# Performance work log

Hardware: AMD Instinct MI355X
Metric: run time of the kernel (lower is better)

Reference implementation:

```python
import jax, jax.numpy as jnp
import numpy as np

LN_EPS = 1e-5


def setup_inputs() -> dict:
    key = jax.random.key(0)
    ks = jax.random.split(key, 4)
    B, D, N = 256, 1024, 100000
    scale = 1.0 / np.sqrt(D)
    return {
        "query": jax.random.normal(ks[0], (B, D), dtype=jnp.float32),
        "W1": jax.random.normal(ks[1], (D, D), dtype=jnp.float32) * scale,
        "b1": jnp.zeros((D,), dtype=jnp.float32),
        "ln_g": jnp.ones((D,), dtype=jnp.float32),
        "ln_b": jnp.zeros((D,), dtype=jnp.float32),
        "W2": jax.random.normal(ks[2], (D, D), dtype=jnp.float32) * scale,
        "b2": jnp.zeros((D,), dtype=jnp.float32),
        "memory": jax.random.normal(ks[3], (N, D), dtype=jnp.float32),
        "k": 16,
    }


def _l2norm(x):
    # F.normalize(p=2, dim=-1): x / max(||x||, eps) with eps=1e-12
    n = jnp.sqrt(jnp.sum(x * x, axis=-1, keepdims=True))
    return x / jnp.maximum(n, 1e-12)


def _layernorm(x, g, b):
    mu = jnp.mean(x, axis=-1, keepdims=True)
    var = jnp.mean((x - mu) ** 2, axis=-1, keepdims=True)
    return (x - mu) * jax.lax.rsqrt(var + LN_EPS) * g + b


def reference(query, W1, b1, ln_g, ln_b, W2, b2, memory, k):
    # project(): Linear -> LayerNorm -> GELU (exact) -> Linear -> L2 normalize
    h = query @ W1.T + b1                      # [B, D]
    h = _layernorm(h, ln_g, ln_b)
    h = jax.nn.gelu(h, approximate=False)
    refined = _l2norm(h @ W2.T + b2)           # [B, D]

    # retrieve_similar(): cosine sims against normalized memory bank, then top-k
    mem_n = _l2norm(memory)                    # [N, D]
    sims = refined @ mem_n.T                   # [B, N]
    topk_vals, topk_idx = jax.lax.top_k(sims, k)   # [B, k]
    retrieved = mem_n[topk_idx]                # [B, k, D] gather
    return refined, topk_vals, topk_idx, retrieved
```

## Files before the change

kernel.cpp:

```cpp
#include <hip/hip_runtime.h>
#include <float.h>
#include <math.h>

#define D 1024
#define BQ 256
#define NMEM 100000
#define TOPK 16
#define NT_TOT 1563

typedef __attribute__((ext_vector_type(4))) float f32x4;
typedef __attribute__((ext_vector_type(8))) short s16x8;

__device__ __forceinline__ void mfma16(f32x4& d, s16x8 a, s16x8 b) {
  asm("v_mfma_f32_16x16x32_bf16 %0, %1, %2, %0" : "+v"(d) : "v"(a), "v"(b));
}

__device__ __forceinline__ unsigned short bf16rtne(float x) {
  unsigned u = __float_as_uint(x);
  unsigned r = u + 0x7fffu + ((u >> 16) & 1u);
  return (unsigned short)(r >> 16);
}

__device__ __forceinline__ void cvt8(float4 a, float4 b, s16x8* hi, s16x8* lo,
                                     float* ssq) {
  float xs[8] = {a.x, a.y, a.z, a.w, b.x, b.y, b.z, b.w};
  union { s16x8 v; unsigned short u[8]; } H, L;
#pragma unroll
  for (int e = 0; e < 8; ++e) {
    float x = xs[e];
    unsigned short h = bf16rtne(x);
    float hf = __uint_as_float(((unsigned)h) << 16);
    H.u[e] = (short)h;
    L.u[e] = (short)bf16rtne(x - hf);
    *ssq = fmaf(x, x, *ssq);
  }
  *hi = H.v;
  *lo = L.v;
}


__device__ __forceinline__ float waveReduceSum(float v) {
#pragma unroll
  for (int o = 32; o > 0; o >>= 1) v += __shfl_xor(v, o, 64);
  return v;
}

__device__ __forceinline__ float blockReduceSum(float v, float* sbuf) {
  v = waveReduceSum(v);
  int w = threadIdx.x >> 6;
  if ((threadIdx.x & 63) == 0) sbuf[w] = v;
  __syncthreads();
  float r = sbuf[0] + sbuf[1] + sbuf[2] + sbuf[3];
  __syncthreads();
  return r;
}


__global__ __launch_bounds__(256) void prep_bf16_kernel(
    const float* __restrict__ src, float* __restrict__ dst, int R16) {
  int g = blockIdx.x * 256 + threadIdx.x;
  int l = g & 63;
  int mt = (g >> 6) % R16;
  int kb = (g >> 6) / R16;
  int row = mt * 16 + (l & 15);
  int k0 = kb * 32 + ((l >> 4) << 3);
  const float* s = src + (size_t)row * D + k0;
  float4 v0 = *(const float4*)s;
  float4 v1 = *(const float4*)(s + 4);
  float xs[8] = {v0.x, v0.y, v0.z, v0.w, v1.x, v1.y, v1.z, v1.w};
  union { uint4 q; unsigned short u[8]; } H, L;
#pragma unroll
  for (int e = 0; e < 8; ++e) {
    float x = xs[e];
    unsigned short h = bf16rtne(x);
    float hf = __uint_as_float(((unsigned)h) << 16);
    H.u[e] = h;
    L.u[e] = bf16rtne(x - hf);
  }
  char* db = (char*)dst + (size_t)kb * (R16 * 2048) + mt * 2048 + l * 16;
  *(uint4*)db = H.q;
  *(uint4*)(db + 1024) = L.q;
}


__global__ __launch_bounds__(256) void mfma_gemm_kernel(
    const float* __restrict__ Afr, const float* __restrict__ Wfr,
    float* __restrict__ part) {
  int t = threadIdx.x;
  int w = t >> 6, l = t & 63;
  int ct = blockIdx.x & 63;
  int kc = blockIdx.x >> 6;
  f32x4 acc[4];
  f32x4 zz = {0.f, 0.f, 0.f, 0.f};
#pragma unroll
  for (int mi = 0; mi < 4; ++mi) acc[mi] = zz;
  const char* ab0 = (const char*)Afr + w * 8192 + l * 16;
  const char* bb0 = (const char*)Wfr + ct * 2048 + l * 16;
#pragma unroll 2
  for (int s = 0; s < 8; ++s) {
    int kb = kc * 8 + s;
    const char* bb = bb0 + (size_t)kb * 131072;
    s16x8 bh = *(const s16x8*)(bb);
    s16x8 bl = *(const s16x8*)(bb + 1024);
    const char* ab = ab0 + (size_t)kb * 32768;
#pragma unroll
    for (int mi = 0; mi < 4; ++mi) {
      s16x8 ah = *(const s16x8*)(ab + mi * 2048);
      s16x8 al = *(const s16x8*)(ab + mi * 2048 + 1024);
      mfma16(acc[mi], ah, bh);
      mfma16(acc[mi], ah, bl);
      mfma16(acc[mi], al, bh);
    }
  }
  float* pb = part + (size_t)kc * 262144 + ct * 16 + (l & 15);
#pragma unroll
  for (int mi = 0; mi < 4; ++mi)
#pragma unroll
    for (int j = 0; j < 4; ++j) {
      int row = w * 64 + mi * 16 + ((l >> 4) << 2) + j;
      pb[(size_t)row * 1024] = acc[mi][j];
    }
}


__global__ __launch_bounds__(256) void reduce_ln_gelu_kernel(
    const float* __restrict__ part, const float* __restrict__ bias,
    const float* __restrict__ g, const float* __restrict__ b,
    float* __restrict__ Hf) {
  __shared__ float sbuf[4];
  int row = blockIdx.x, t = threadIdx.x;
  const float* p = part + (size_t)row * 1024 + t * 4;
  float4 x0 = *(const float4*)(p);
  float4 x1 = *(const float4*)(p + 262144);
  float4 x2 = *(const float4*)(p + 524288);
  float4 x3 = *(const float4*)(p + 786432);
  float4 bb = *(const float4*)(bias + t * 4);
  float vx = x0.x + x1.x + x2.x + x3.x + bb.x;
  float vy = x0.y + x1.y + x2.y + x3.y + bb.y;
  float vz = x0.z + x1.z + x2.z + x3.z + bb.z;
  float vw = x0.w + x1.w + x2.w + x3.w + bb.w;
  float s = blockReduceSum(vx + vy + vz + vw, sbuf);
  float mu = s * (1.0f / D);
  float dx = vx - mu, dy = vy - mu, dz = vz - mu, dw = vw - mu;
  float ss = blockReduceSum(dx * dx + dy * dy + dz * dz + dw * dw, sbuf);
  float rstd = rsqrtf(ss * (1.0f / D) + 1e-5f);
  float4 gg = *(const float4*)(g + t * 4);
  float4 be = *(const float4*)(b + t * 4);
  float y[4];
  y[0] = dx * rstd * gg.x + be.x;
  y[1] = dy * rstd * gg.y + be.y;
  y[2] = dz * rstd * gg.z + be.z;
  y[3] = dw * rstd * gg.w + be.w;
  const float c = 0.70710678118654752f;
  union { uint2 q; unsigned short u[4]; } H, L;
#pragma unroll
  for (int e = 0; e < 4; ++e) {
    float ye = 0.5f * y[e] * (1.0f + erff(y[e] * c));
    unsigned short h = bf16rtne(ye);
    float hf = __uint_as_float(((unsigned)h) << 16);
    H.u[e] = h;
    L.u[e] = bf16rtne(ye - hf);
  }
  int kb = t >> 3, oct = (t >> 1) & 3;
  char* db = (char*)Hf + (size_t)kb * 32768 + (row >> 4) * 2048 +
             ((row & 15) + oct * 16) * 16 + (t & 1) * 8;
  *(uint2*)db = H.q;
  *(uint2*)(db + 1024) = L.q;
}


__global__ __launch_bounds__(256) void reduce_l2norm_kernel(
    const float* __restrict__ part, const float* __restrict__ bias,
    float* __restrict__ outRef, float* __restrict__ Af) {
  __shared__ float sbuf[4];
  int row = blockIdx.x, t = threadIdx.x;
  const float* p = part + (size_t)row * 1024 + t * 4;
  float4 x0 = *(const float4*)(p);
  float4 x1 = *(const float4*)(p + 262144);
  float4 x2 = *(const float4*)(p + 524288);
  float4 x3 = *(const float4*)(p + 786432);
  float4 bb = *(const float4*)(bias + t * 4);
  float vx = x0.x + x1.x + x2.x + x3.x + bb.x;
  float vy = x0.y + x1.y + x2.y + x3.y + bb.y;
  float vz = x0.z + x1.z + x2.z + x3.z + bb.z;
  float vw = x0.w + x1.w + x2.w + x3.w + bb.w;
  float ss = blockReduceSum(vx * vx + vy * vy + vz * vz + vw * vw, sbuf);
  float inv = 1.0f / fmaxf(sqrtf(ss), 1e-12f);
  float y[4] = {vx * inv, vy * inv, vz * inv, vw * inv};
  *(float4*)(outRef + (size_t)row * D + t * 4) =
      make_float4(y[0], y[1], y[2], y[3]);
  union { uint2 q; unsigned short u[4]; } H, L;
#pragma unroll
  for (int e = 0; e < 4; ++e) {
    unsigned short h = bf16rtne(y[e]);
    float hf = __uint_as_float(((unsigned)h) << 16);
    H.u[e] = h;
    L.u[e] = bf16rtne(y[e] - hf);
  }
  int kb = t >> 3, oct = (t >> 1) & 3;
  char* db = (char*)Af + (size_t)kb * 32768 + (row >> 4) * 2048 +
             ((row & 15) + oct * 16) * 16 + (t & 1) * 8;
  *(uint2*)db = H.q;
  *(uint2*)(db + 1024) = L.q;
}

__global__ void zero_ctrs_kernel(int* c) { c[threadIdx.x] = 0; }


#define SBODY(J, BP, ACh, ACl, ANh, ANl, RC0, RC1, RP0, RP1, DOPFB, DOPFA,    \
              DOCONV)                                                          \
  do {                                                                         \
    if (DOCONV) {                                                              \
      s16x8 bhn_, bln_;                                                        \
      cvt8(RC0, RC1, &bhn_, &bln_, &ssq);                                      \
      char* bw_ = smem + (1 - (BP)) * 8192 + bwoff;                            \
      *(s16x8*)bw_ = bhn_;                                                     \
      *(s16x8*)(bw_ + 1024) = bln_;                                            \
    }                                                                          \
    if (DOPFA) {                                                               \
      const char* an_ = afbytes + (size_t)((J) + 1) * 32768 + w4x + l * 16;    \
      _Pragma("unroll") for (int mi = 0; mi < 4; ++mi) {                       \
        ANh[mi] = *(const s16x8*)(an_ + mi * 2048);                            \
        ANl[mi] = *(const s16x8*)(an_ + mi * 2048 + 1024);                     \
      }                                                                        \
    }                                                                          \
    if (DOPFB) {                                                               \
      const float* p_ = bsrc + ((J) + 3) * 32;                                 \
      RP0 = *(const float4*)p_;                                                \
      RP1 = *(const float4*)(p_ + 4);                                          \
    }                                                                          \
    __builtin_amdgcn_s_setprio(1);                                             \
    _Pragma("unroll") for (int ni = 0; ni < 4; ++ni) {                         \
      const char* bb_ = smem + (BP)*8192 + ni * 2048 + l * 16;                 \
      s16x8 bh_ = *(const s16x8*)bb_;                                          \
      s16x8 bl_ = *(const s16x8*)(bb_ + 1024);                                 \
      _Pragma("unroll") for (int mi = 0; mi < 4; ++mi) {                       \
        mfma16(acc[mi][ni], ACh[mi], bh_);                                     \
        mfma16(acc[mi][ni], ACh[mi], bl_);                                     \
        mfma16(acc[mi][ni], ACl[mi], bh_);                                     \
      }                                                                        \
    }                                                                          \
    __builtin_amdgcn_s_setprio(0);                                             \
    asm volatile("s_waitcnt lgkmcnt(0)\n\ts_barrier" ::: "memory");            \
    __builtin_amdgcn_sched_barrier(0);                                         \
  } while (0)

__global__ __launch_bounds__(256, 2) void sims_gemm_kernel(
    const float* __restrict__ Afrag, const float* __restrict__ mem,
    float* __restrict__ invn, int* __restrict__ ctr,
    float* __restrict__ simsbuf, int ntiles, int chunk_n0, int stride_cols) {
  __shared__ __align__(16) char smem[16384];
  __shared__ float sInvF[64];
  __shared__ int s_tile;
  const int t = threadIdx.x;
  const int w = t >> 6, l = t & 63;
  const int w4x = (w * 4) * 2048;
  const int brow_loc = t >> 2;
  const int kseg = t & 3;
  const int bwoff = (brow_loc >> 4) * 2048 + ((brow_loc & 15) + kseg * 16) * 16;
  const char* afbytes = (const char*)Afrag;

  while (true) {
    if (t == 0) s_tile = atomicAdd(ctr, 1);
    __syncthreads();
    const int unit = s_tile;
    __syncthreads();
    if (unit >= ntiles) break;
    const int n0 = chunk_n0 + unit * 64;
    const int brow = min(n0 + brow_loc, NMEM - 1);
    const float* bsrc = mem + (size_t)brow * D + kseg * 8;

    f32x4 acc[4][4];
    f32x4 zz = {0.f, 0.f, 0.f, 0.f};
#pragma unroll
    for (int mi = 0; mi < 4; ++mi)
#pragma unroll
      for (int ni = 0; ni < 4; ++ni) acc[mi][ni] = zz;
    float ssq = 0.f;

    float4 r0a, r0b, r1a, r1b, r2a, r2b;
    s16x8 s0h[4], s0l[4], s1h[4], s1l[4];

    r0a = *(const float4*)bsrc;
    r0b = *(const float4*)(bsrc + 4);
    r1a = *(const float4*)(bsrc + 32);
    r1b = *(const float4*)(bsrc + 36);
    r2a = *(const float4*)(bsrc + 64);
    r2b = *(const float4*)(bsrc + 68);
    {
      const char* a0_ = afbytes + w4x + l * 16;
#pragma unroll
      for (int mi = 0; mi < 4; ++mi) {
        s0h[mi] = *(const s16x8*)(a0_ + mi * 2048);
        s0l[mi] = *(const s16x8*)(a0_ + mi * 2048 + 1024);
      }
    }
    {
      s16x8 bh0, bl0;
      cvt8(r0a, r0b, &bh0, &bl0, &ssq);
      *(s16x8*)(smem + bwoff) = bh0;
      *(s16x8*)(smem + bwoff + 1024) = bl0;
    }
    asm volatile("s_waitcnt lgkmcnt(0)\n\ts_barrier" ::: "memory");
    __builtin_amdgcn_sched_barrier(0);

#pragma unroll 1
    for (int jb = 0; jb < 24; jb += 6) {
      SBODY(jb + 0, 0, s0h, s0l, s1h, s1l, r1a, r1b, r0a, r0b, 1, 1, 1);
      SBODY(jb + 1, 1, s1h, s1l, s0h, s0l, r2a, r2b, r1a, r1b, 1, 1, 1);
      SBODY(jb + 2, 0, s0h, s0l, s1h, s1l, r0a, r0b, r2a, r2b, 1, 1, 1);
      SBODY(jb + 3, 1, s1h, s1l, s0h, s0l, r1a, r1b, r0a, r0b, 1, 1, 1);
      SBODY(jb + 4, 0, s0h, s0l, s1h, s1l, r2a, r2b, r1a, r1b, 1, 1, 1);
      SBODY(jb + 5, 1, s1h, s1l, s0h, s0l, r0a, r0b, r2a, r2b, 1, 1, 1);
    }
    SBODY(24, 0, s0h, s0l, s1h, s1l, r1a, r1b, r0a, r0b, 1, 1, 1);
    SBODY(25, 1, s1h, s1l, s0h, s0l, r2a, r2b, r1a, r1b, 1, 1, 1);
    SBODY(26, 0, s0h, s0l, s1h, s1l, r0a, r0b, r2a, r2b, 1, 1, 1);
    SBODY(27, 1, s1h, s1l, s0h, s0l, r1a, r1b, r0a, r0b, 1, 1, 1);
    SBODY(28, 0, s0h, s0l, s1h, s1l, r2a, r2b, r1a, r1b, 1, 1, 1);
    SBODY(29, 1, s1h, s1l, s0h, s0l, r0a, r0b, r2a, r2b, 0, 1, 1);
    SBODY(30, 0, s0h, s0l, s1h, s1l, r1a, r1b, r0a, r0b, 0, 1, 1);
    SBODY(31, 1, s1h, s1l, s0h, s0l, r2a, r2b, r1a, r1b, 0, 0, 0);

    float s2 = ssq + __shfl_xor(ssq, 1, 64);
    s2 = s2 + __shfl_xor(s2, 2, 64);
    float inv = 1.0f / fmaxf(sqrtf(s2), 1e-12f);
    if (kseg == 0) {
      sInvF[brow_loc] = inv;
      int col = n0 + brow_loc;
      if (col < NMEM) invn[col] = inv;
    }
    __syncthreads();
    float siv[4];
#pragma unroll
    for (int ni = 0; ni < 4; ++ni) siv[ni] = sInvF[ni * 16 + (l & 15)];
    float* srow = simsbuf + (size_t)(unit * 64);
#pragma unroll
    for (int mi = 0; mi < 4; ++mi)
#pragma unroll
      for (int jj = 0; jj < 4; ++jj) {
        int row = w * 64 + mi * 16 + ((l >> 4) << 2) + jj;
        float* rp = srow + (size_t)row * stride_cols;
#pragma unroll
        for (int ni = 0; ni < 4; ++ni)
          rp[ni * 16 + (l & 15)] = acc[mi][ni][jj] * siv[ni];
      }
    __syncthreads();
  }
}


__global__ __launch_bounds__(512) void topk_chunk_kernel(
    const float* __restrict__ simsbuf, int stride_cols, int chunk_n0,
    int nvalid, float* __restrict__ cv, int* __restrict__ ci) {
  __shared__ float wvv[8];
  __shared__ int wii[8];
  __shared__ float sbv;
  __shared__ int sbi;
  int row = blockIdx.x, t = threadIdx.x;
  const float* S = simsbuf + (size_t)row * stride_cols;
  float tv[16];
  int ti[16];
#pragma unroll
  for (int s = 0; s < 16; ++s) { tv[s] = -FLT_MAX; ti[s] = 2147483647; }
  float curMin = -FLT_MAX;
  for (int c0 = t * 4; c0 < nvalid; c0 += 2048) {
    float vv[4] = {-FLT_MAX, -FLT_MAX, -FLT_MAX, -FLT_MAX};
    if (c0 + 4 <= nvalid) {
      float4 v = *(const float4*)(S + c0);
      vv[0] = v.x; vv[1] = v.y; vv[2] = v.z; vv[3] = v.w;
    } else {
#pragma unroll
      for (int e = 0; e < 4; ++e)
        if (c0 + e < nvalid) vv[e] = S[c0 + e];
    }
#pragma unroll
    for (int e = 0; e < 4; ++e) {
      float v = vv[e];
      if (v > curMin) {
        int n = chunk_n0 + c0 + e;
        int ms = 0;
        float mv = tv[0];
#pragma unroll
        for (int s = 1; s < 16; ++s)
          if (tv[s] < mv) { mv = tv[s]; ms = s; }
#pragma unroll
        for (int s = 0; s < 16; ++s)
          if (s == ms) { tv[s] = v; ti[s] = n; }
        curMin = tv[0];
#pragma unroll
        for (int s = 1; s < 16; ++s) curMin = fminf(curMin, tv[s]);
      }
    }
  }
  float lastV = FLT_MAX;
  int lastI = -1;
  for (int pass = 0; pass < TOPK; ++pass) {
    float bv = -FLT_MAX;
    int bi = 2147483647;
#pragma unroll
    for (int s = 0; s < 16; ++s) {
      float v = tv[s];
      int idx = ti[s];
      bool qual = (v < lastV) || (v == lastV && idx > lastI);
      bool bet = (v > bv) || (v == bv && idx < bi);
      if (qual && bet) { bv = v; bi = idx; }
    }
#pragma unroll
    for (int o = 32; o > 0; o >>= 1) {
      float v2 = __shfl_xor(bv, o, 64);
      int i2 = __shfl_xor(bi, o, 64);
      if (v2 > bv || (v2 == bv && i2 < bi)) { bv = v2; bi = i2; }
    }
    if ((t & 63) == 0) { wvv[t >> 6] = bv; wii[t >> 6] = bi; }
    __syncthreads();
    if (t == 0) {
      float fv = wvv[0];
      int fi = wii[0];
#pragma unroll
      for (int u = 1; u < 8; ++u) {
        if (wvv[u] > fv || (wvv[u] == fv && wii[u] < fi)) {
          fv = wvv[u];
          fi = wii[u];
        }
      }
      sbv = fv;
      sbi = fi;
      cv[row * TOPK + pass] = fv;
      ci[row * TOPK + pass] = fi;
    }
    __syncthreads();
    lastV = sbv;
    lastI = sbi;
  }
}


__global__ __launch_bounds__(64) void final_merge_kernel(
    const float* __restrict__ cand_v, const int* __restrict__ cand_i,
    int nchunk, float* __restrict__ out_vals, float* __restrict__ out_idx) {
  int row = blockIdx.x, l = threadIdx.x;
  int nc = nchunk * TOPK;
  float mv[8];
  int mi_[8];
#pragma unroll
  for (int u = 0; u < 8; ++u) {
    int p = l + u * 64;
    if (p < nc) {
      int ch = p >> 4;
      mv[u] = cand_v[ch * 4096 + row * TOPK + (p & 15)];
      mi_[u] = cand_i[ch * 4096 + row * TOPK + (p & 15)];
    } else {
      mv[u] = -FLT_MAX;
      mi_[u] = 2147483647;
    }
  }
  float lastV = FLT_MAX;
  int lastI = -1;
  for (int pass = 0; pass < TOPK; ++pass) {
    float bv = -FLT_MAX;
    int bi = 2147483647;
#pragma unroll
    for (int u = 0; u < 8; ++u) {
      bool qual = (mv[u] < lastV) || (mv[u] == lastV && mi_[u] > lastI);
      bool bet = (mv[u] > bv) || (mv[u] == bv && mi_[u] < bi);
      if (qual && bet) { bv = mv[u]; bi = mi_[u]; }
    }
#pragma unroll
    for (int o = 32; o > 0; o >>= 1) {
      float v2 = __shfl_xor(bv, o, 64);
      int i2 = __shfl_xor(bi, o, 64);
      if (v2 > bv || (v2 == bv && i2 < bi)) { bv = v2; bi = i2; }
    }
    bv = __shfl(bv, 0, 64);
    bi = __shfl(bi, 0, 64);
    if (l == 0) {
      out_vals[row * TOPK + pass] = bv;
      out_idx[row * TOPK + pass] = (float)bi;
    }
    lastV = bv;
    lastI = bi;
  }
}


__global__ __launch_bounds__(256) void gather_kernel(
    const float* __restrict__ out_idx, const float* __restrict__ mem,
    const float* __restrict__ invn, float* __restrict__ out_retr) {
  int p = blockIdx.x;
  int idx = (int)out_idx[p];
  float inv = invn[idx];
  int c = threadIdx.x * 4;
  float4 v = *(const float4*)(mem + (size_t)idx * D + c);
  v.x *= inv; v.y *= inv; v.z *= inv; v.w *= inv;
  *(float4*)(out_retr + (size_t)p * D + c) = v;
}


extern "C" void kernel_launch(void* const* d_in, const int* in_sizes, int n_in,
                              void* d_out, int out_size, void* d_ws,
                              size_t ws_size, hipStream_t stream) {
  const float* query = (const float*)d_in[0];
  const float* W1 = (const float*)d_in[1];
  const float* b1 = (const float*)d_in[2];
  const float* ln_g = (const float*)d_in[3];
  const float* ln_b = (const float*)d_in[4];
  const float* W2 = (const float*)d_in[5];
  const float* b2 = (const float*)d_in[6];
  const float* mem = (const float*)d_in[7];

  float* out = (float*)d_out;
  float* out_refined = out;
  float* out_vals = out + 262144;
  float* out_idx = out + 262144 + 4096;
  float* out_retr = out + 262144 + 8192;

  float* wsp = (float*)d_ws;
  float* invn = wsp;
  float* Qf = wsp + 100352;
  float* Af = wsp + 362496;
  float* W1f = wsp + 624640;
  float* W2f = wsp + 1673216;
  float* part = wsp + 2721792;
  float* cand_v = wsp + 3770368;
  int* cand_i = (int*)(wsp + 3901440);
  int* ctrs = (int*)(wsp + 4032512);
  float* sims = wsp + 4032576;

  long ws_floats = (long)(ws_size / 4);
  long avail = ws_floats - 4032640;
  int tpc = (int)(avail / 16384);
  if (tpc > NT_TOT) tpc = NT_TOT;
  if (tpc < 1) tpc = 1;
  int nchunk = (NT_TOT + tpc - 1) / tpc;
  if (nchunk > 32) nchunk = 32;
  tpc = (NT_TOT + nchunk - 1) / nchunk;
  int stride = tpc * 64;

  zero_ctrs_kernel<<<1, 64, 0, stream>>>(ctrs);
  prep_bf16_kernel<<<128, 256, 0, stream>>>(query, Qf, 16);
  prep_bf16_kernel<<<512, 256, 0, stream>>>(W1, W1f, 64);
  prep_bf16_kernel<<<512, 256, 0, stream>>>(W2, W2f, 64);
  mfma_gemm_kernel<<<256, 256, 0, stream>>>(Qf, W1f, part);
  reduce_ln_gelu_kernel<<<256, 256, 0, stream>>>(part, b1, ln_g, ln_b, Qf);
  mfma_gemm_kernel<<<256, 256, 0, stream>>>(Qf, W2f, part);
  reduce_l2norm_kernel<<<256, 256, 0, stream>>>(part, b2, out_refined, Af);
  for (int c = 0; c < nchunk; ++c) {
    int t0 = c * tpc;
    int nt = NT_TOT - t0;
    if (nt > tpc) nt = tpc;
    if (nt <= 0) break;
    int base = t0 * 64;
    sims_gemm_kernel<<<512, 256, 0, stream>>>(Af, mem, invn, ctrs + c, sims,
                                              nt, base, stride);
    int nvalid = NMEM - base;
    if (nvalid > nt * 64) nvalid = nt * 64;
    topk_chunk_kernel<<<256, 512, 0, stream>>>(sims, stride, base, nvalid,
                                               cand_v + c * 4096,
                                               cand_i + c * 4096);
  }
  final_merge_kernel<<<256, 64, 0, stream>>>(cand_v, cand_i, nchunk, out_vals,
                                             out_idx);
  gather_kernel<<<BQ * TOPK, 256, 0, stream>>>(out_idx, mem, invn, out_retr);
}
```

Baseline: 414.4 us.

## Split per-row top-k scan into segments and double sims GEMM grid

The chunk top-k kernel can now split each row's column range into several segments, each handled by its own block, giving 4x more blocks when there are few chunks. The final merge then combines the extra candidate lists. The sims GEMM launch also goes from 512 to 1024 blocks. The aim is to fill more CUs during the top-k scan and the GEMM, at the cost of more candidates to merge and more blocks contending on the work counters.

```diff
diff --git a/kernel.cpp b/kernel.cpp
--- a/kernel.cpp
+++ b/kernel.cpp
@@ -7,6 +7,7 @@
 #define NMEM 100000
 #define TOPK 16
 #define NT_TOT 1563
+#define SIMS_BLOCKS 1024
 
 typedef __attribute__((ext_vector_type(4))) float f32x4;
 typedef __attribute__((ext_vector_type(8))) short s16x8;
@@ -352,27 +353,32 @@
 
 __global__ __launch_bounds__(512) void topk_chunk_kernel(
     const float* __restrict__ simsbuf, int stride_cols, int chunk_n0,
-    int nvalid, float* __restrict__ cv, int* __restrict__ ci) {
+    int nvalid, int seglen, float* __restrict__ cv, int* __restrict__ ci) {
   __shared__ float wvv[8];
   __shared__ int wii[8];
   __shared__ float sbv;
   __shared__ int sbi;
-  int row = blockIdx.x, t = threadIdx.x;
+  int row = blockIdx.x & 255;
+  int seg = blockIdx.x >> 8;
+  int c0beg = seg * seglen;
+  int c0end = c0beg + seglen;
+  if (c0end > nvalid) c0end = nvalid;
+  int t = threadIdx.x;
   const float* S = simsbuf + (size_t)row * stride_cols;
   float tv[16];
   int ti[16];
 #pragma unroll
   for (int s = 0; s < 16; ++s) { tv[s] = -FLT_MAX; ti[s] = 2147483647; }
   float curMin = -FLT_MAX;
-  for (int c0 = t * 4; c0 < nvalid; c0 += 2048) {
+  for (int c0 = c0beg + t * 4; c0 < c0end; c0 += 2048) {
     float vv[4] = {-FLT_MAX, -FLT_MAX, -FLT_MAX, -FLT_MAX};
-    if (c0 + 4 <= nvalid) {
+    if (c0 + 4 <= c0end) {
       float4 v = *(const float4*)(S + c0);
       vv[0] = v.x; vv[1] = v.y; vv[2] = v.z; vv[3] = v.w;
     } else {
 #pragma unroll
       for (int e = 0; e < 4; ++e)
-        if (c0 + e < nvalid) vv[e] = S[c0 + e];
+        if (c0 + e < c0end) vv[e] = S[c0 + e];
     }
 #pragma unroll
     for (int e = 0; e < 4; ++e) {
@@ -426,8 +432,8 @@
       }
       sbv = fv;
       sbi = fi;
-      cv[row * TOPK + pass] = fv;
-      ci[row * TOPK + pass] = fi;
+      cv[seg * 4096 + row * TOPK + pass] = fv;
+      ci[seg * 4096 + row * TOPK + pass] = fi;
     }
     __syncthreads();
     lastV = sbv;
@@ -438,9 +444,9 @@
 
 __global__ __launch_bounds__(64) void final_merge_kernel(
     const float* __restrict__ cand_v, const int* __restrict__ cand_i,
-    int nchunk, float* __restrict__ out_vals, float* __restrict__ out_idx) {
+    int nlists, float* __restrict__ out_vals, float* __restrict__ out_idx) {
   int row = blockIdx.x, l = threadIdx.x;
-  int nc = nchunk * TOPK;
+  int nc = nlists * TOPK;
   float mv[8];
   int mi_[8];
 #pragma unroll
@@ -536,6 +542,7 @@
   if (nchunk > 32) nchunk = 32;
   tpc = (NT_TOT + nchunk - 1) / nchunk;
   int stride = tpc * 64;
+  int nseg = (nchunk <= 8) ? 4 : 1;
 
   zero_ctrs_kernel<<<1, 64, 0, stream>>>(ctrs);
   prep_bf16_kernel<<<128, 256, 0, stream>>>(query, Qf, 16);
@@ -551,15 +558,16 @@
     if (nt > tpc) nt = tpc;
     if (nt <= 0) break;
     int base = t0 * 64;
-    sims_gemm_kernel<<<512, 256, 0, stream>>>(Af, mem, invn, ctrs + c, sims,
-                                              nt, base, stride);
+    sims_gemm_kernel<<<SIMS_BLOCKS, 256, 0, stream>>>(Af, mem, invn, ctrs + c,
+                                                      sims, nt, base, stride);
     int nvalid = NMEM - base;
     if (nvalid > nt * 64) nvalid = nt * 64;
-    topk_chunk_kernel<<<256, 512, 0, stream>>>(sims, stride, base, nvalid,
-                                               cand_v + c * 4096,
-                                               cand_i + c * 4096);
-  }
-  final_merge_kernel<<<256, 64, 0, stream>>>(cand_v, cand_i, nchunk, out_vals,
-                                             out_idx);
+    int seglen = ((nvalid + nseg - 1) / nseg + 3) & ~3;
+    topk_chunk_kernel<<<256 * nseg, 512, 0, stream>>>(
+        sims, stride, base, nvalid, seglen, cand_v + c * nseg * 4096,
+        cand_i + c * nseg * 4096);
+  }
+  final_merge_kernel<<<256, 64, 0, stream>>>(cand_v, cand_i, nchunk * nseg,
+                                             out_vals, out_idx);
   gather_kernel<<<BQ * TOPK, 256, 0, stream>>>(out_idx, mem, invn, out_retr);
 }
```

After: 415.1 us. No clear change (+0.2%).
